# Optimization experiments

Measured on AMD Instinct MI355X. Metric: run time of the kernel, lower is better.

## Reference

```python
import jax, jax.numpy as jnp
import numpy as np

VOCAB = 100000
HIDDEN = 512
NUM_CLUSTERS = 256
B, S = 8, 2048


def setup_inputs() -> dict:
    key = jax.random.key(0)
    k1, k2, k3, k4, k5 = jax.random.split(key, 5)
    return {
        "location_ids": jax.random.randint(k1, (B, S), 0, VOCAB),
        "fine_embed_w": jax.random.normal(k2, (VOCAB, HIDDEN // 2), dtype=jnp.float32),
        "coarse_embed_w": jax.random.normal(k3, (NUM_CLUSTERS, HIDDEN // 2), dtype=jnp.float32),
        "loc_to_cluster_w": jax.random.normal(k4, (NUM_CLUSTERS, VOCAB), dtype=jnp.float32),
        "loc_to_cluster_b": jax.random.normal(k5, (NUM_CLUSTERS,), dtype=jnp.float32),
    }


def reference(location_ids, fine_embed_w, coarse_embed_w, loc_to_cluster_w, loc_to_cluster_b):
    # fine embedding gather: [B,S,H/2]
    fine_emb = fine_embed_w[location_ids]
    # one_hot(ids) @ W^T + b  ==  gather columns of W at ids, plus bias
    # cluster_logits: [B,S,C]
    cluster_logits = loc_to_cluster_w.T[location_ids] + loc_to_cluster_b
    cluster_dist = jax.nn.softmax(cluster_logits, axis=-1)
    # soft mixture of coarse cluster embeddings: [B,S,H/2]
    coarse_emb = jnp.einsum("bsc,ch->bsh", cluster_dist, coarse_embed_w)
    return jnp.concatenate([fine_emb, coarse_emb], axis=-1)
```

## Files before the change

### kernel.cpp

```cpp
#include <hip/hip_runtime.h>
#include <hip/hip_bf16.h>

#define VOCAB 100000
#define HALF  256
#define NC    256
#define NTOK  16384
#define NBUCK 2048
#define SEGSZ 3200
#define NSEG  32
#define BPS   50

using frag  = __attribute__((ext_vector_type(8))) short;
using f32x4 = __attribute__((ext_vector_type(4))) float;

static __device__ inline unsigned bfpk(float lo, float hi) {
    union { __hip_bfloat162 h2; unsigned u; } cv;
    cv.h2.x = __float2bfloat16(lo);
    cv.h2.y = __float2bfloat16(hi);
    return cv.u;
}

__global__ __launch_bounds__(1024)
void zero_hist(int* __restrict__ hist) {
    hist[blockIdx.x * 1024 + threadIdx.x] = 0;
}

__global__ __launch_bounds__(1024)
void hist_kernel(const int* __restrict__ ids, int* __restrict__ hist) {
    const int t = blockIdx.x * 1024 + threadIdx.x;
    atomicAdd(&hist[ids[t] >> 6], 1);
}

__global__ __launch_bounds__(1024)
void scan_kernel(const int* __restrict__ hist, int* __restrict__ offs,
                 int* __restrict__ bexcl) {
    __shared__ int part[1024];
    const int tid = threadIdx.x;
    const int h0 = hist[2 * tid], h1 = hist[2 * tid + 1];
    part[tid] = h0 + h1;
    __syncthreads();
    for (int off = 1; off < 1024; off <<= 1) {
        const int v   = part[tid];
        const int add = (tid >= off) ? part[tid - off] : 0;
        __syncthreads();
        part[tid] = v + add;
        __syncthreads();
    }
    const int excl = (tid == 0) ? 0 : part[tid - 1];
    offs[2 * tid]      = excl;
    offs[2 * tid + 1]  = excl + h0;
    bexcl[2 * tid]     = excl;
    bexcl[2 * tid + 1] = excl + h0;
}

__global__ __launch_bounds__(1024)
void scatter_kernel(const int* __restrict__ ids, int* __restrict__ offs,
                    int* __restrict__ stok, int* __restrict__ sidv) {
    const int t = blockIdx.x * 1024 + threadIdx.x;
    const int id = ids[t];
    const int pos = atomicAdd(&offs[id >> 6], 1);
    stok[pos] = t;
    sidv[pos] = id;
}

__global__ __launch_bounds__(256)
void coarse_T(const float* __restrict__ cw, ushort* __restrict__ cT) {
    const int h = blockIdx.x;
    const int c = threadIdx.x;
    __hip_bfloat16 b = __float2bfloat16(cw[c * HALF + h]);
    cT[h * NC + c] = *reinterpret_cast<ushort*>(&b);
}

__global__ __launch_bounds__(256)
void gather_rows(const float* __restrict__ cluster_w,
                 const float* __restrict__ cluster_b,
                 const int*   __restrict__ sidv,
                 const int*   __restrict__ bexcl,
                 __hip_bfloat16* __restrict__ logT)
{
    __shared__ float seg[SEGSZ];
    const int bid = blockIdx.x;
    const int r   = bid >> 5;
    const int s   = bid & 31;
    const int tid = threadIdx.x;
    const int sbase = s * SEGSZ;
    const int slen  = min(SEGSZ, VOCAB - sbase);

    const float4* src = reinterpret_cast<const float4*>(cluster_w + (size_t)r * VOCAB + sbase);
    float4* dst = reinterpret_cast<float4*>(seg);
    const int nf4 = slen >> 2;
    for (int i = tid; i < nf4; i += 256) dst[i] = src[i];

    const float bias = cluster_b[r];
    const int lo = bexcl[s * BPS];
    const int hi = bexcl[(s + 1) * BPS];
    __syncthreads();

    for (int i = lo + tid; i < hi; i += 256) {
        const int id = sidv[i];
        logT[(size_t)r * NTOK + i] = __float2bfloat16(seg[id - sbase] + bias);
    }
}

__global__ __launch_bounds__(512)
void mix_mfma(const ushort* __restrict__ logT,
              const float*  __restrict__ fine_w,
              const ushort* __restrict__ cT,
              const int*    __restrict__ stok,
              const int*    __restrict__ sidv,
              float*        __restrict__ out)
{
    __shared__ uint4 ldsA[32][33];
    __shared__ uint4 ldsB[256][5];
    __shared__ float redu[32][17];
    __shared__ int stok_l[32], sid_l[32];

    const int tid  = threadIdx.x;
    const int base = blockIdx.x * 32;

    if (tid < 32) { stok_l[tid] = stok[base + tid]; sid_l[tid] = sidv[base + tid]; }

    const int s = tid & 31;
    const int g = tid >> 5;
    float v[16];
#pragma unroll
    for (int i = 0; i < 16; ++i) {
        const unsigned u = logT[(size_t)(g * 16 + i) * NTOK + base + s];
        v[i] = __uint_as_float(u << 16);
    }
    float m = v[0];
#pragma unroll
    for (int i = 1; i < 16; ++i) m = fmaxf(m, v[i]);
    redu[s][g] = m;
    __syncthreads();
    float M = redu[s][0];
#pragma unroll
    for (int i = 1; i < 16; ++i) M = fmaxf(M, redu[s][i]);
    __syncthreads();
    float sum = 0.f;
#pragma unroll
    for (int i = 0; i < 16; ++i) { v[i] = __expf(v[i] - M); sum += v[i]; }
    redu[s][g] = sum;
    __syncthreads();
    float tot = 0.f;
#pragma unroll
    for (int i = 0; i < 16; ++i) tot += redu[s][i];
    const float inv = 1.f / tot;

    {
        uint4 u0, u1;
        u0.x = bfpk(v[0] * inv,  v[1] * inv);
        u0.y = bfpk(v[2] * inv,  v[3] * inv);
        u0.z = bfpk(v[4] * inv,  v[5] * inv);
        u0.w = bfpk(v[6] * inv,  v[7] * inv);
        u1.x = bfpk(v[8] * inv,  v[9] * inv);
        u1.y = bfpk(v[10] * inv, v[11] * inv);
        u1.z = bfpk(v[12] * inv, v[13] * inv);
        u1.w = bfpk(v[14] * inv, v[15] * inv);
        ldsA[s][2 * g]     = u0;
        ldsA[s][2 * g + 1] = u1;
    }

    {
        const int sl = tid >> 4, l16 = tid & 15;
        const float4* fs = reinterpret_cast<const float4*>(fine_w + (size_t)sid_l[sl] * HALF);
        float4* fd = reinterpret_cast<float4*>(out + (size_t)stok_l[sl] * 512);
#pragma unroll
        for (int p = 0; p < 4; ++p) fd[l16 + 16 * p] = fs[l16 + 16 * p];
    }

    const int w    = tid >> 6;
    const int lane = tid & 63;
    const int arow = (w & 1) * 16 + (lane & 15);
    const int ngrp = (w >> 1) * 4;
    f32x4 acc[4];
#pragma unroll
    for (int q = 0; q < 4; ++q) acc[q] = (f32x4){0.f, 0.f, 0.f, 0.f};

    for (int ch = 0; ch < 8; ++ch) {
        __syncthreads();
#pragma unroll
        for (int p = 0; p < 2; ++p) {
            const int idx = tid + p * 512;
            const int n = idx >> 2, kb2 = idx & 3;
            ldsB[n][kb2] = *reinterpret_cast<const uint4*>(cT + (size_t)n * NC + ch * 32 + kb2 * 8);
        }
        __syncthreads();

        const frag a = *reinterpret_cast<const frag*>(&ldsA[arow][ch * 4 + (lane >> 4)]);
#pragma unroll
        for (int q = 0; q < 4; ++q) {
            const int nt = ngrp + q;
            const frag b = *reinterpret_cast<const frag*>(&ldsB[nt * 16 + (lane & 15)][lane >> 4]);
            acc[q] = __builtin_amdgcn_mfma_f32_16x16x32_bf16(a, b, acc[q], 0, 0, 0);
        }
    }

#pragma unroll
    for (int q = 0; q < 4; ++q) {
        const int col = (ngrp + q) * 16 + (lane & 15);
#pragma unroll
        for (int r = 0; r < 4; ++r) {
            const int srow = (w & 1) * 16 + (lane >> 4) * 4 + r;
            out[(size_t)stok_l[srow] * 512 + 256 + col] = acc[q][r];
        }
    }
}

extern "C" void kernel_launch(void* const* d_in, const int* in_sizes, int n_in,
                              void* d_out, int out_size, void* d_ws, size_t ws_size,
                              hipStream_t stream) {
    const int*   ids       = (const int*)  d_in[0];
    const float* fine_w    = (const float*)d_in[1];
    const float* coarse_w  = (const float*)d_in[2];
    const float* cluster_w = (const float*)d_in[3];
    const float* cluster_b = (const float*)d_in[4];
    float*       out       = (float*)d_out;

    int* offs  = (int*)d_ws;
    int* hist  = offs + NBUCK;
    int* bexcl = hist + NBUCK;
    int* stok  = bexcl + NBUCK;
    int* sidv  = stok + NTOK;
    __hip_bfloat16* logT = (__hip_bfloat16*)(sidv + NTOK);
    ushort* cT = (ushort*)(logT + (size_t)NC * NTOK);

    const size_t need = (size_t)(3 * NBUCK + 2 * NTOK) * sizeof(int)
                      + (size_t)NC * NTOK * 2 + (size_t)HALF * NC * 2;
    if (ws_size < need) return;

    hipLaunchKernelGGL(zero_hist,      dim3(NBUCK / 1024), dim3(1024), 0, stream, hist);
    hipLaunchKernelGGL(coarse_T,       dim3(HALF),         dim3(256),  0, stream, coarse_w, cT);
    hipLaunchKernelGGL(hist_kernel,    dim3(NTOK / 1024),  dim3(1024), 0, stream, ids, hist);
    hipLaunchKernelGGL(scan_kernel,    dim3(1),            dim3(1024), 0, stream, hist, offs, bexcl);
    hipLaunchKernelGGL(scatter_kernel, dim3(NTOK / 1024),  dim3(1024), 0, stream, ids, offs, stok, sidv);
    hipLaunchKernelGGL(gather_rows,    dim3(NC * NSEG),    dim3(256),  0, stream,
                       cluster_w, cluster_b, sidv, bexcl, logT);
    hipLaunchKernelGGL(mix_mfma,       dim3(NTOK / 32),    dim3(512),  0, stream,
                       (const ushort*)logT, fine_w, cT, stok, sidv, out);
}
```

Before: 58.97 us.

## Fuse bucket-sort prep kernels and read coarse weights directly from global

Merges zero/hist/scan/scatter/transpose into two kernels: prep1 computes per-block LDS histograms alongside a tiled coarse-weight transpose, and prep2 redundantly scans partial histograms per block and scatters using LDS atomics. This cuts kernel launches and global atomics. Separately, mix_mfma drops the LDS staging of cT and its per-chunk barriers, loading B fragments straight from global/L2 instead. That trades fewer barriers for more redundant global reads across blocks.

```diff
diff --git a/kernel.cpp b/kernel.cpp
--- a/kernel.cpp
+++ b/kernel.cpp
@@ -9,6 +9,7 @@
 #define SEGSZ 3200
 #define NSEG  32
 #define BPS   50
+#define NHB   16
 
 using frag  = __attribute__((ext_vector_type(8))) short;
 using f32x4 = __attribute__((ext_vector_type(4))) float;
@@ -21,54 +22,95 @@
 }
 
 __global__ __launch_bounds__(1024)
-void zero_hist(int* __restrict__ hist) {
-    hist[blockIdx.x * 1024 + threadIdx.x] = 0;
+void prep1(const int* __restrict__ ids, const float* __restrict__ coarse_w,
+           int* __restrict__ partial, ushort* __restrict__ cT)
+{
+    __shared__ float tile[64][65];
+    __shared__ int lh[NBUCK];
+    const int tid = threadIdx.x;
+    const int b   = blockIdx.x;
+
+    if (b < NHB) {
+        lh[tid] = 0; lh[tid + 1024] = 0;
+        __syncthreads();
+        atomicAdd(&lh[ids[b * 1024 + tid] >> 6], 1);
+        __syncthreads();
+        partial[b * NBUCK + tid]        = lh[tid];
+        partial[b * NBUCK + tid + 1024] = lh[tid + 1024];
+    } else {
+        const int bt = b - NHB;
+        const int ci = (bt >> 2) * 64, hi = (bt & 3) * 64;
+#pragma unroll
+        for (int p = 0; p < 4; ++p) {
+            const int idx = tid + p * 1024;
+            const int cl = idx >> 6, hl = idx & 63;
+            tile[cl][hl] = coarse_w[(size_t)(ci + cl) * HALF + hi + hl];
+        }
+        __syncthreads();
+#pragma unroll
+        for (int p = 0; p < 4; ++p) {
+            const int idx = tid + p * 1024;
+            const int hl = idx >> 6, cl = idx & 63;
+            __hip_bfloat16 v = __float2bfloat16(tile[cl][hl]);
+            cT[(size_t)(hi + hl) * NC + ci + cl] = *reinterpret_cast<ushort*>(&v);
+        }
+    }
 }
 
 __global__ __launch_bounds__(1024)
-void hist_kernel(const int* __restrict__ ids, int* __restrict__ hist) {
-    const int t = blockIdx.x * 1024 + threadIdx.x;
-    atomicAdd(&hist[ids[t] >> 6], 1);
-}
-
-__global__ __launch_bounds__(1024)
-void scan_kernel(const int* __restrict__ hist, int* __restrict__ offs,
-                 int* __restrict__ bexcl) {
-    __shared__ int part[1024];
+void prep2(const int* __restrict__ ids, const int* __restrict__ partial,
+           int* __restrict__ bexcl, int* __restrict__ stok, int* __restrict__ sidv)
+{
+    __shared__ int A_[NBUCK], B_[NBUCK], base_[NBUCK], lcnt_[NBUCK];
     const int tid = threadIdx.x;
-    const int h0 = hist[2 * tid], h1 = hist[2 * tid + 1];
-    part[tid] = h0 + h1;
-    __syncthreads();
-    for (int off = 1; off < 1024; off <<= 1) {
-        const int v   = part[tid];
-        const int add = (tid >= off) ? part[tid - off] : 0;
-        __syncthreads();
-        part[tid] = v + add;
-        __syncthreads();
-    }
-    const int excl = (tid == 0) ? 0 : part[tid - 1];
-    offs[2 * tid]      = excl;
-    offs[2 * tid + 1]  = excl + h0;
-    bexcl[2 * tid]     = excl;
-    bexcl[2 * tid + 1] = excl + h0;
-}
-
-__global__ __launch_bounds__(1024)
-void scatter_kernel(const int* __restrict__ ids, int* __restrict__ offs,
-                    int* __restrict__ stok, int* __restrict__ sidv) {
-    const int t = blockIdx.x * 1024 + threadIdx.x;
+    const int b   = blockIdx.x;
+
+#pragma unroll
+    for (int p = 0; p < 2; ++p) {
+        const int e = tid + p * 1024;
+        int tot = 0, bas = 0;
+#pragma unroll
+        for (int bb = 0; bb < NHB; ++bb) {
+            const int v = partial[bb * NBUCK + e];
+            tot += v;
+            if (bb < b) bas += v;
+        }
+        A_[e] = tot; base_[e] = bas; lcnt_[e] = 0;
+    }
+    __syncthreads();
+
+    int* src = A_; int* dst = B_;
+    for (int off = 1; off < NBUCK; off <<= 1) {
+#pragma unroll
+        for (int p = 0; p < 2; ++p) {
+            const int e = tid + p * 1024;
+            dst[e] = src[e] + (e >= off ? src[e - off] : 0);
+        }
+        __syncthreads();
+        int* tmp = src; src = dst; dst = tmp;
+    }
+#pragma unroll
+    for (int p = 0; p < 2; ++p) {
+        const int e = tid + p * 1024;
+        dst[e] = e ? src[e - 1] : 0;
+    }
+    __syncthreads();
+
+    if (b == 0) {
+#pragma unroll
+        for (int p = 0; p < 2; ++p) {
+            const int e = tid + p * 1024;
+            bexcl[e] = dst[e];
+        }
+    }
+
+    const int t  = b * 1024 + tid;
     const int id = ids[t];
-    const int pos = atomicAdd(&offs[id >> 6], 1);
+    const int k  = id >> 6;
+    const int r  = atomicAdd(&lcnt_[k], 1);
+    const int pos = dst[k] + base_[k] + r;
     stok[pos] = t;
     sidv[pos] = id;
-}
-
-__global__ __launch_bounds__(256)
-void coarse_T(const float* __restrict__ cw, ushort* __restrict__ cT) {
-    const int h = blockIdx.x;
-    const int c = threadIdx.x;
-    __hip_bfloat16 b = __float2bfloat16(cw[c * HALF + h]);
-    cT[h * NC + c] = *reinterpret_cast<ushort*>(&b);
 }
 
 __global__ __launch_bounds__(256)
@@ -111,7 +153,6 @@
               float*        __restrict__ out)
 {
     __shared__ uint4 ldsA[32][33];
-    __shared__ uint4 ldsB[256][5];
     __shared__ float redu[32][17];
     __shared__ int stok_l[32], sid_l[32];
 
@@ -168,6 +209,7 @@
 #pragma unroll
         for (int p = 0; p < 4; ++p) fd[l16 + 16 * p] = fs[l16 + 16 * p];
     }
+    __syncthreads();
 
     const int w    = tid >> 6;
     const int lane = tid & 63;
@@ -178,20 +220,12 @@
     for (int q = 0; q < 4; ++q) acc[q] = (f32x4){0.f, 0.f, 0.f, 0.f};
 
     for (int ch = 0; ch < 8; ++ch) {
-        __syncthreads();
-#pragma unroll
-        for (int p = 0; p < 2; ++p) {
-            const int idx = tid + p * 512;
-            const int n = idx >> 2, kb2 = idx & 3;
-            ldsB[n][kb2] = *reinterpret_cast<const uint4*>(cT + (size_t)n * NC + ch * 32 + kb2 * 8);
-        }
-        __syncthreads();
-
         const frag a = *reinterpret_cast<const frag*>(&ldsA[arow][ch * 4 + (lane >> 4)]);
 #pragma unroll
         for (int q = 0; q < 4; ++q) {
-            const int nt = ngrp + q;
-            const frag b = *reinterpret_cast<const frag*>(&ldsB[nt * 16 + (lane & 15)][lane >> 4]);
+            const int n = (ngrp + q) * 16 + (lane & 15);
+            const frag b = *reinterpret_cast<const frag*>(
+                cT + (size_t)n * NC + ch * 32 + (lane >> 4) * 8);
             acc[q] = __builtin_amdgcn_mfma_f32_16x16x32_bf16(a, b, acc[q], 0, 0, 0);
         }
     }
@@ -217,25 +251,23 @@
     const float* cluster_b = (const float*)d_in[4];
     float*       out       = (float*)d_out;
 
-    int* offs  = (int*)d_ws;
-    int* hist  = offs + NBUCK;
-    int* bexcl = hist + NBUCK;
-    int* stok  = bexcl + NBUCK;
-    int* sidv  = stok + NTOK;
+    int* partial = (int*)d_ws;
+    int* bexcl   = partial + NHB * NBUCK;
+    int* stok    = bexcl + NBUCK;
+    int* sidv    = stok + NTOK;
     __hip_bfloat16* logT = (__hip_bfloat16*)(sidv + NTOK);
     ushort* cT = (ushort*)(logT + (size_t)NC * NTOK);
 
-    const size_t need = (size_t)(3 * NBUCK + 2 * NTOK) * sizeof(int)
+    const size_t need = (size_t)(NHB * NBUCK + NBUCK + 2 * NTOK) * sizeof(int)
                       + (size_t)NC * NTOK * 2 + (size_t)HALF * NC * 2;
     if (ws_size < need) return;
 
-    hipLaunchKernelGGL(zero_hist,      dim3(NBUCK / 1024), dim3(1024), 0, stream, hist);
-    hipLaunchKernelGGL(coarse_T,       dim3(HALF),         dim3(256),  0, stream, coarse_w, cT);
-    hipLaunchKernelGGL(hist_kernel,    dim3(NTOK / 1024),  dim3(1024), 0, stream, ids, hist);
-    hipLaunchKernelGGL(scan_kernel,    dim3(1),            dim3(1024), 0, stream, hist, offs, bexcl);
-    hipLaunchKernelGGL(scatter_kernel, dim3(NTOK / 1024),  dim3(1024), 0, stream, ids, offs, stok, sidv);
-    hipLaunchKernelGGL(gather_rows,    dim3(NC * NSEG),    dim3(256),  0, stream,
+    hipLaunchKernelGGL(prep1, dim3(2 * NHB), dim3(1024), 0, stream,
+                       ids, coarse_w, partial, cT);
+    hipLaunchKernelGGL(prep2, dim3(NHB), dim3(1024), 0, stream,
+                       ids, partial, bexcl, stok, sidv);
+    hipLaunchKernelGGL(gather_rows, dim3(NC * NSEG), dim3(256), 0, stream,
                        cluster_w, cluster_b, sidv, bexcl, logT);
-    hipLaunchKernelGGL(mix_mfma,       dim3(NTOK / 32),    dim3(512),  0, stream,
+    hipLaunchKernelGGL(mix_mfma, dim3(NTOK / 32), dim3(512), 0, stream,
                        (const ushort*)logT, fine_w, cT, stok, sidv, out);
 }
```

Measured after the change: 58.36 us. Within noise of the previous version (-1.0%).
